# Performance work log

Measured on AMD Instinct MI355X. Metric: run time of the kernel, lower is better.

The kernel has to match this reference:

```python
import jax, jax.numpy as jnp
import numpy as np
import math

E = 512
H = 2048
P = 128  # attention_limit

def _make_params(key):
    ks = jax.random.split(key, 6)
    s = 0.02
    p = {}
    p['wq'] = jax.random.normal(ks[0], (E, E), jnp.float32) * s
    p['bq'] = jnp.zeros((E,), jnp.float32)
    p['wk'] = jax.random.normal(ks[1], (E, E), jnp.float32) * s
    p['bk'] = jnp.zeros((E,), jnp.float32)
    p['wv'] = jax.random.normal(ks[2], (E, E), jnp.float32) * s
    p['bv'] = jnp.zeros((E,), jnp.float32)
    p['w1'] = jax.random.normal(ks[3], (E, H), jnp.float32) * s
    p['b1'] = jnp.zeros((H,), jnp.float32)
    p['w2'] = jax.random.normal(ks[4], (H, E), jnp.float32) * s
    p['b2'] = jnp.zeros((E,), jnp.float32)
    p['ln1_w'] = jnp.ones((E,), jnp.float32)
    p['ln1_b'] = jnp.zeros((E,), jnp.float32)
    p['ln2_w'] = jnp.ones((E,), jnp.float32)
    p['ln2_b'] = jnp.zeros((E,), jnp.float32)
    return p

def setup_inputs() -> dict:
    key = jax.random.key(0)
    kx, kp = jax.random.split(key)
    inp = {'x': jax.random.normal(kx, (2, 1024, E), jnp.float32)}
    inp.update(_make_params(kp))
    return inp

def _layernorm(x, w, b, eps=1e-5):
    mu = jnp.mean(x, axis=-1, keepdims=True)
    var = jnp.mean((x - mu) ** 2, axis=-1, keepdims=True)
    return (x - mu) / jnp.sqrt(var + eps) * w + b

def _forward(x, wq, bq, wk, bk, wv, bv, w1, b1, w2, b2, ln1_w, ln1_b, ln2_w, ln2_b):
    B, S, Ed = x.shape
    # "RoPE" is actually additive sinusoidal PE in the source
    pos = jnp.arange(S, dtype=jnp.float32)[:, None]
    div = jnp.exp(jnp.arange(0, Ed, 2, dtype=jnp.float32) * (-math.log(10000.0) / Ed))
    pe = jnp.zeros((S, Ed), jnp.float32)
    pe = pe.at[:, 0::2].set(jnp.sin(pos * div))
    pe = pe.at[:, 1::2].set(jnp.cos(pos * div))
    x = x + pe[None]

    # local attention: pad x first, then apply K/V linears (padded rows -> bias)
    x_ext = jnp.pad(x, ((0, 0), (P, P), (0, 0)))
    q = x @ wq + bq                      # [B,S,E]
    k_ext = x_ext @ wk + bk              # [B,S+2P,E]
    v_ext = x_ext @ wv + bv
    W = 2 * P + 1
    win_idx = jnp.arange(S)[:, None] + jnp.arange(W)[None, :]  # [S,W]
    k_win = k_ext[:, win_idx]            # [B,S,W,E]
    v_win = v_ext[:, win_idx]            # [B,S,W,E]
    energy = jnp.einsum('bse,bswe->bsw', q, k_win) / jnp.sqrt(jnp.float32(Ed))
    attn = jax.nn.softmax(energy, axis=-1)
    attn_out = jnp.einsum('bsw,bswe->bse', attn, v_win)

    x = _layernorm(attn_out + x, ln1_w, ln1_b)
    ff = jnp.maximum(x @ w1 + b1, 0.0) @ w2 + b2
    return _layernorm(ff + x, ln2_w, ln2_b)

def reference(x, wq, bq, wk, bk, wv, bv, w1, b1, w2, b2, ln1_w, ln1_b, ln2_w, ln2_b):
    return _forward(x, wq, bq, wk, bk, wv, bv, w1, b1, w2, b2, ln1_w, ln1_b, ln2_w, ln2_b)
```

## Files before the change

### kernel.cpp

```cpp
#include <hip/hip_runtime.h>
#include <hip/hip_bf16.h>

#define S_LEN 1024
#define E_DIM 512
#define H_DIM 2048
#define P_PAD 128
#define EXTA 1296
#define BS_ROWS 2048

typedef __attribute__((ext_vector_type(8))) short bf16x8;
typedef __attribute__((ext_vector_type(4))) float f32x4;

__device__ inline ushort f2bf(float x) {
  union { float f; unsigned u; } c; c.f = x;
  unsigned u = c.u;
  u += 0x7fffu + ((u >> 16) & 1u);
  return (ushort)(u >> 16);
}

__device__ inline void gload16(ushort* dst, const ushort* src) {
  __builtin_amdgcn_global_load_lds(
      (const __attribute__((address_space(1))) void*)src,
      (__attribute__((address_space(3))) void*)dst, 16, 0, 0);
}

__global__ __launch_bounds__(256) void prep_kernel(const float* __restrict__ x,
                                                   const float* __restrict__ bk,
                                                   const float* __restrict__ bv,
                                                   const float* __restrict__ wq,
                                                   const float* __restrict__ wk,
                                                   const float* __restrict__ wv,
                                                   const float* __restrict__ w1,
                                                   const float* __restrict__ w2,
                                                   float* __restrict__ xpe,
                                                   ushort* __restrict__ xpe_bf,
                                                   ushort* __restrict__ k_bf,
                                                   ushort* __restrict__ v_t,
                                                   ushort* __restrict__ wqkvT,
                                                   ushort* __restrict__ w1T,
                                                   ushort* __restrict__ w2T) {
  __shared__ float t[32][33];
  const int blk = blockIdx.x;
  if (blk < 4096) {
    int idx = blk * 256 + threadIdx.x;
    int e = idx & (E_DIM - 1);
    int s = (idx >> 9) & (S_LEN - 1);
    const float c = -9.210340371976184f / 512.0f;
    float freq = expf((float)(e & ~1) * c);
    float ang = (float)s * freq;
    float pe = (e & 1) ? cosf(ang) : sinf(ang);
    float v = x[idx] + pe;
    xpe[idx] = v;
    xpe_bf[idx] = f2bf(v);
  } else if (blk < 6272) {
    int p = (blk - 4096) * 256 + threadIdx.x;
    int t2 = p / (2 * 272 * 512);
    int r2 = p % (2 * 272 * 512);
    int b = r2 / (272 * 512);
    int r3 = r2 % (272 * 512);
    if (t2 == 0) {
      int rr = r3 >> 9, e = r3 & 511;
      int row = rr < 128 ? rr : 1024 + rr;
      float v = rr < 256 ? bk[e] : 0.f;
      k_bf[((size_t)b * EXTA + row) * 512 + e] = f2bf(v);
    } else {
      int n = r3 / 272, jj = r3 % 272;
      int j = jj < 128 ? jj : 1024 + jj;
      float v = jj < 256 ? bv[n] : 0.f;
      v_t[((size_t)b * 512 + n) * EXTA + j] = f2bf(v);
    }
  } else {
    const int tile = blk - 6272;
    const float* W; ushort* WT; int K, N, bx, by;
    if (tile < 768) {
      K = 512; N = 512;
      int sect = tile >> 8, tt = tile & 255;
      W = sect == 0 ? wq : (sect == 1 ? wk : wv);
      WT = wqkvT + (size_t)sect * 512 * 512;
      bx = tt & 15; by = tt >> 4;
    } else if (tile < 1792) {
      K = 512; N = 2048; W = w1; WT = w1T;
      int tt = tile - 768; bx = tt & 63; by = tt >> 6;
    } else {
      K = 2048; N = 512; W = w2; WT = w2T;
      int tt = tile - 1792; bx = tt & 15; by = tt >> 4;
    }
    int lx = threadIdx.x & 31, ly = threadIdx.x >> 5;
    int n0 = bx * 32, k0 = by * 32;
#pragma unroll
    for (int r = 0; r < 4; ++r)
      t[ly + r * 8][lx] = W[(size_t)(k0 + ly + r * 8) * N + n0 + lx];
    __syncthreads();
#pragma unroll
    for (int r = 0; r < 4; ++r)
      WT[(size_t)(n0 + ly + r * 8) * K + k0 + lx] = f2bf(t[lx][ly + r * 8]);
  }
}

template <int BM, int BN, int WM, int WN, int OUT>
__global__ __launch_bounds__(256) void mfma_gemm(const ushort* __restrict__ A,
                                                 const ushort* __restrict__ Bt,
                                                 const float* __restrict__ bias,
                                                 const float* __restrict__ bias2,
                                                 const float* __restrict__ bias3,
                                                 void* __restrict__ Cout,
                                                 ushort* __restrict__ q_out,
                                                 ushort* __restrict__ k_out,
                                                 ushort* __restrict__ v_out,
                                                 int M, int N, int K, int LDA) {
  constexpr int WAVES_N = BN / WN;
  constexpr int FM = WM / 16, FN = WN / 16;
  __shared__ ushort As[BM * 64];
  __shared__ ushort Bs[BN * 64];
  const int tid = threadIdx.x;
  const int lane = tid & 63;
  const int w = tid >> 6;
  const int wr = w / WAVES_N, wc = w % WAVES_N;
  const int l15 = lane & 15, lhi = lane >> 4;
  const int col0 = blockIdx.x * BN, row0 = blockIdx.y * BM;
  const int koff = blockIdx.z * K;

  f32x4 acc[FM][FN] = {};

  for (int k0 = 0; k0 < K; k0 += 64) {
#pragma unroll
    for (int it = 0; it < BM / 32; ++it) {
      int u = it * 256 + tid;
      int r = u >> 3;
      int c16 = (u & 7) ^ (r & 7);
      gload16(&As[(size_t)u * 8], &A[(size_t)(row0 + r) * LDA + koff + k0 + c16 * 8]);
    }
#pragma unroll
    for (int it = 0; it < BN / 32; ++it) {
      int u = it * 256 + tid;
      int r = u >> 3;
      int c16 = (u & 7) ^ (r & 7);
      gload16(&Bs[(size_t)u * 8], &Bt[(size_t)(col0 + r) * LDA + koff + k0 + c16 * 8]);
    }
    __syncthreads();
#pragma unroll
    for (int kk = 0; kk < 2; ++kk) {
      bf16x8 af[FM], bfr[FN];
#pragma unroll
      for (int mi = 0; mi < FM; ++mi) {
        int r = wr * WM + mi * 16 + l15;
        int c16 = (kk * 4 + lhi) ^ (r & 7);
        af[mi] = *(const bf16x8*)&As[r * 64 + c16 * 8];
      }
#pragma unroll
      for (int ni = 0; ni < FN; ++ni) {
        int r = wc * WN + ni * 16 + l15;
        int c16 = (kk * 4 + lhi) ^ (r & 7);
        bfr[ni] = *(const bf16x8*)&Bs[r * 64 + c16 * 8];
      }
#pragma unroll
      for (int mi = 0; mi < FM; ++mi)
#pragma unroll
        for (int ni = 0; ni < FN; ++ni)
          acc[mi][ni] = __builtin_amdgcn_mfma_f32_16x16x32_bf16(af[mi], bfr[ni], acc[mi][ni], 0, 0, 0);
    }
    __syncthreads();
  }

#pragma unroll
  for (int mi = 0; mi < FM; ++mi) {
    int mbase = row0 + wr * WM + mi * 16 + lhi * 4;
#pragma unroll
    for (int ni = 0; ni < FN; ++ni) {
      int n = col0 + wc * WN + ni * 16 + l15;
      if constexpr (OUT == 1) {
        float b = bias[n];
        ushort* C = (ushort*)Cout;
#pragma unroll
        for (int j = 0; j < 4; ++j) C[(size_t)(mbase + j) * N + n] = f2bf(fmaxf(acc[mi][ni][j] + b, 0.f));
      } else if constexpr (OUT == 3) {
        float* C = (float*)Cout + (size_t)blockIdx.z * M * N;
#pragma unroll
        for (int j = 0; j < 4; ++j) C[(size_t)(mbase + j) * N + n] = acc[mi][ni][j];
      } else {
        int sect = n >> 9, nn = n & 511;
        float b = sect == 0 ? bias[nn] : (sect == 1 ? bias2[nn] : bias3[nn]);
        int bb = mbase >> 10;
        int s = mbase & 1023;
        if (sect == 0) {
#pragma unroll
          for (int j = 0; j < 4; ++j) q_out[(size_t)(mbase + j) * 512 + nn] = f2bf(acc[mi][ni][j] + b);
        } else if (sect == 1) {
#pragma unroll
          for (int j = 0; j < 4; ++j)
            k_out[((size_t)bb * EXTA + 128 + s + j) * 512 + nn] = f2bf(acc[mi][ni][j] + b);
        } else {
          ushort4 pk;
          pk.x = f2bf(acc[mi][ni][0] + b);
          pk.y = f2bf(acc[mi][ni][1] + b);
          pk.z = f2bf(acc[mi][ni][2] + b);
          pk.w = f2bf(acc[mi][ni][3] + b);
          *(ushort4*)&v_out[((size_t)bb * 512 + nn) * EXTA + 128 + s] = pk;
        }
      }
    }
  }
}

__global__ __launch_bounds__(512) void attn_ln1(const ushort* __restrict__ qb,
                                                const ushort* __restrict__ kb,
                                                const ushort* __restrict__ vt,
                                                const float* __restrict__ x_pe,
                                                const float* __restrict__ ln1w,
                                                const float* __restrict__ ln1b,
                                                float* __restrict__ x1,
                                                ushort* __restrict__ x1bf) {
  __shared__ float e_s[16][292];
  __shared__ ushort p_s[16][296];
  __shared__ float inv_s[16];
  __shared__ float redS[8][16];
  __shared__ float redQ[8][16];
  __shared__ float mu_s[16], rs_s[16];
  const int tid = threadIdx.x;
  const int lane = tid & 63;
  const int w = tid >> 6;
  const int l15 = lane & 15, lhi = lane >> 4;
  const int tile = blockIdx.x;
  const int b = tile >> 6;
  const int s0 = (tile & 63) * 16;
  const int base0 = b * 1024 + s0;

  const ushort* qrow = qb + (size_t)(base0 + l15) * 512 + lhi * 8;
  bf16x8 qf[16];
#pragma unroll
  for (int ks = 0; ks < 16; ++ks) qf[ks] = *(const bf16x8*)(qrow + ks * 32);

  const float scale = 0.044194173824159216f;
  const ushort* kbase = kb + (size_t)b * EXTA * 512 + (size_t)(s0 + l15) * 512 + lhi * 8;

  for (int jt = w; jt < 18; jt += 8) {
    f32x4 acc = {};
    const ushort* kp = kbase + (size_t)jt * 16 * 512;
#pragma unroll
    for (int ks = 0; ks < 16; ++ks) {
      bf16x8 kf = *(const bf16x8*)(kp + ks * 32);
      acc = __builtin_amdgcn_mfma_f32_16x16x32_bf16(qf[ks], kf, acc, 0, 0, 0);
    }
    int jc = jt * 16 + l15;
#pragma unroll
    for (int j = 0; j < 4; ++j) {
      int i = lhi * 4 + j;
      bool valid = (jc >= i) && (jc <= i + 256);
      e_s[i][jc] = valid ? acc[j] * scale : -1e30f;
    }
  }
  __syncthreads();

  {
    int r = tid >> 5, c0 = tid & 31;
    float m = -1e30f;
#pragma unroll
    for (int t = 0; t < 9; ++t) m = fmaxf(m, e_s[r][c0 + 32 * t]);
#pragma unroll
    for (int off = 1; off <= 16; off <<= 1) m = fmaxf(m, __shfl_xor(m, off));
    float s = 0.f;
#pragma unroll
    for (int t = 0; t < 9; ++t) {
      float p = __expf(e_s[r][c0 + 32 * t] - m);
      s += p;
      p_s[r][c0 + 32 * t] = f2bf(p);
    }
#pragma unroll
    for (int off = 1; off <= 16; off <<= 1) s += __shfl_xor(s, off);
    if (c0 == 0) inv_s[r] = 1.0f / s;
  }
  __syncthreads();

  bf16x8 pf[9];
#pragma unroll
  for (int ks = 0; ks < 9; ++ks) pf[ks] = *(const bf16x8*)&p_s[l15][ks * 32 + lhi * 8];
  float inv[4];
#pragma unroll
  for (int j = 0; j < 4; ++j) inv[j] = inv_s[lhi * 4 + j];

  const ushort* vbase = vt + (size_t)b * 512 * EXTA + s0 + lhi * 8;
  float val[4][4];
#pragma unroll
  for (int ni = 0; ni < 4; ++ni) {
    int n = w * 64 + ni * 16 + l15;
    f32x4 acc = {};
    const ushort* vp = vbase + (size_t)n * EXTA;
#pragma unroll
    for (int ks = 0; ks < 9; ++ks) {
      bf16x8 vf = *(const bf16x8*)(vp + ks * 32);
      acc = __builtin_amdgcn_mfma_f32_16x16x32_bf16(pf[ks], vf, acc, 0, 0, 0);
    }
#pragma unroll
    for (int j = 0; j < 4; ++j) {
      int r = lhi * 4 + j;
      val[ni][j] = acc[j] * inv[j] + x_pe[(size_t)(base0 + r) * 512 + n];
    }
  }

  float S[4], Q[4];
#pragma unroll
  for (int j = 0; j < 4; ++j) {
    S[j] = 0.f; Q[j] = 0.f;
#pragma unroll
    for (int ni = 0; ni < 4; ++ni) { S[j] += val[ni][j]; Q[j] += val[ni][j] * val[ni][j]; }
  }
#pragma unroll
  for (int off = 1; off <= 8; off <<= 1) {
#pragma unroll
    for (int j = 0; j < 4; ++j) {
      S[j] += __shfl_xor(S[j], off);
      Q[j] += __shfl_xor(Q[j], off);
    }
  }
  if (l15 == 0) {
#pragma unroll
    for (int j = 0; j < 4; ++j) { redS[w][lhi * 4 + j] = S[j]; redQ[w][lhi * 4 + j] = Q[j]; }
  }
  __syncthreads();
  if (tid < 16) {
    float sS = 0.f, sQ = 0.f;
#pragma unroll
    for (int ww = 0; ww < 8; ++ww) { sS += redS[ww][tid]; sQ += redQ[ww][tid]; }
    float mu = sS * (1.0f / 512.0f);
    float var = sQ * (1.0f / 512.0f) - mu * mu;
    mu_s[tid] = mu;
    rs_s[tid] = rsqrtf(var + 1e-5f);
  }
  __syncthreads();

#pragma unroll
  for (int ni = 0; ni < 4; ++ni) {
    int n = w * 64 + ni * 16 + l15;
    float lw = ln1w[n], lb = ln1b[n];
#pragma unroll
    for (int j = 0; j < 4; ++j) {
      int r = lhi * 4 + j;
      float o = (val[ni][j] - mu_s[r]) * rs_s[r] * lw + lb;
      x1[(size_t)(base0 + r) * 512 + n] = o;
      x1bf[(size_t)(base0 + r) * 512 + n] = f2bf(o);
    }
  }
}

__device__ inline float wave_reduce_sum(float v) {
#pragma unroll
  for (int off = 32; off >= 1; off >>= 1) v += __shfl_xor(v, off);
  return v;
}

__global__ __launch_bounds__(256) void ln_kernel(const float* __restrict__ a,
                                                 const float* __restrict__ a2,
                                                 const float* __restrict__ ab,
                                                 const float* __restrict__ rsd,
                                                 const float* __restrict__ w,
                                                 const float* __restrict__ bias,
                                                 float* __restrict__ out) {
  const int row = blockIdx.x;
  const int tid = threadIdx.x;
  __shared__ float red[8];
  const int e0 = tid * 2;
  const size_t base = (size_t)row * E_DIM + e0;
  float2 av = *(const float2*)(a + base);
  float2 rv = *(const float2*)(rsd + base);
  float x0 = av.x + rv.x, x1 = av.y + rv.y;
  {
    float2 v2 = *(const float2*)(a2 + base);
    x0 += v2.x; x1 += v2.y;
  }
  {
    float2 bb = *(const float2*)(ab + e0);
    x0 += bb.x; x1 += bb.y;
  }

  float sm = wave_reduce_sum(x0 + x1);
  if ((tid & 63) == 0) red[tid >> 6] = sm;
  __syncthreads();
  float mu = (red[0] + red[1] + red[2] + red[3]) * (1.0f / 512.0f);
  float d0 = x0 - mu, d1 = x1 - mu;
  float vs = wave_reduce_sum(d0 * d0 + d1 * d1);
  if ((tid & 63) == 0) red[4 + (tid >> 6)] = vs;
  __syncthreads();
  float var = (red[4] + red[5] + red[6] + red[7]) * (1.0f / 512.0f);
  float inv = rsqrtf(var + 1e-5f);
  float2 wv = *(const float2*)(w + e0);
  float2 bi = *(const float2*)(bias + e0);
  float o0 = d0 * inv * wv.x + bi.x;
  float o1 = d1 * inv * wv.y + bi.y;
  *(float2*)(out + base) = make_float2(o0, o1);
}

extern "C" void kernel_launch(void* const* d_in, const int* in_sizes, int n_in,
                              void* d_out, int out_size, void* d_ws, size_t ws_size,
                              hipStream_t stream) {
  const float* x    = (const float*)d_in[0];
  const float* wq   = (const float*)d_in[1];
  const float* bq   = (const float*)d_in[2];
  const float* wk   = (const float*)d_in[3];
  const float* bk   = (const float*)d_in[4];
  const float* wv   = (const float*)d_in[5];
  const float* bv   = (const float*)d_in[6];
  const float* w1   = (const float*)d_in[7];
  const float* b1   = (const float*)d_in[8];
  const float* w2   = (const float*)d_in[9];
  const float* b2   = (const float*)d_in[10];
  const float* ln1w = (const float*)d_in[11];
  const float* ln1b = (const float*)d_in[12];
  const float* ln2w = (const float*)d_in[13];
  const float* ln2b = (const float*)d_in[14];

  char* W = (char*)d_ws;
  float*  x_pe   = (float*)(W);
  ushort* xpebf  = (ushort*)(W + (4u  << 20));
  ushort* wqkvT  = (ushort*)(W + (6u  << 20));
  ushort* w1T    = (ushort*)(W + (8u  << 20));
  ushort* w2T    = (ushort*)(W + (10u << 20));
  ushort* q_bf   = (ushort*)(W + (12u << 20));
  ushort* k_bf   = (ushort*)(W + (14u << 20));
  ushort* v_t    = (ushort*)(W + (17u << 20));
  float*  x1     = (float*)(W + (20u << 20));
  ushort* x1bf   = (ushort*)(W + (24u << 20));
  ushort* ff1_bf = (ushort*)(W + (26u << 20));
  float*  ff2    = (float*)(W + (34u << 20));

  prep_kernel<<<9088, 256, 0, stream>>>(x, bk, bv, wq, wk, wv, w1, w2,
                                        x_pe, xpebf, k_bf, v_t, wqkvT, w1T, w2T);

  mfma_gemm<64, 128, 32, 64, 2><<<dim3(12, 32), 256, 0, stream>>>(
      xpebf, wqkvT, bq, bk, bv, nullptr, q_bf, k_bf, v_t, BS_ROWS, 1536, 512, 512);

  attn_ln1<<<128, 512, 0, stream>>>(q_bf, k_bf, v_t, x_pe, ln1w, ln1b, x1, x1bf);

  mfma_gemm<64, 128, 32, 64, 1><<<dim3(16, 32), 256, 0, stream>>>(
      x1bf, w1T, b1, nullptr, nullptr, ff1_bf, nullptr, nullptr, nullptr, BS_ROWS, H_DIM, 512, 512);

  mfma_gemm<64, 64, 32, 32, 3><<<dim3(8, 32, 2), 256, 0, stream>>>(
      ff1_bf, w2T, nullptr, nullptr, nullptr, ff2, nullptr, nullptr, nullptr, BS_ROWS, E_DIM, 1024, 2048);

  ln_kernel<<<BS_ROWS, 256, 0, stream>>>(ff2, ff2 + (size_t)BS_ROWS * E_DIM, b2, x1,
                                         ln2w, ln2b, (float*)d_out);
}
```

Measured before the change: 77.08 us.

## Fuse all stages into one cooperative persistent kernel with grid syncs

Replaces the six separate launches (prep, QKV GEMM, attention+LN1, FF1 GEMM, FF2 GEMM, LN2) with a single cooperative kernel of 256 blocks of 512 threads that separates phases with grid.sync(). GEMM tiles grow to 128x128, and FF2 is split over four K-slices instead of two, with the final LayerNorm reducing those partials one row per wave. The aim is to remove launch gaps and inter-kernel overhead, at the cost of grid-wide barriers, idle blocks in phases with fewer tiles (QKV uses 192 blocks, attention 128), and a fixed small grid.

```diff
diff --git a/kernel.cpp b/kernel.cpp
--- a/kernel.cpp
+++ b/kernel.cpp
@@ -1,10 +1,12 @@
 #include <hip/hip_runtime.h>
 #include <hip/hip_bf16.h>
+#include <hip/hip_cooperative_groups.h>
+
+namespace cg = cooperative_groups;
 
 #define S_LEN 1024
 #define E_DIM 512
 #define H_DIM 2048
-#define P_PAD 128
 #define EXTA 1296
 #define BS_ROWS 2048
 
@@ -24,157 +26,98 @@
       (__attribute__((address_space(3))) void*)dst, 16, 0, 0);
 }
 
-__global__ __launch_bounds__(256) void prep_kernel(const float* __restrict__ x,
-                                                   const float* __restrict__ bk,
-                                                   const float* __restrict__ bv,
-                                                   const float* __restrict__ wq,
-                                                   const float* __restrict__ wk,
-                                                   const float* __restrict__ wv,
-                                                   const float* __restrict__ w1,
-                                                   const float* __restrict__ w2,
-                                                   float* __restrict__ xpe,
-                                                   ushort* __restrict__ xpe_bf,
-                                                   ushort* __restrict__ k_bf,
-                                                   ushort* __restrict__ v_t,
-                                                   ushort* __restrict__ wqkvT,
-                                                   ushort* __restrict__ w1T,
-                                                   ushort* __restrict__ w2T) {
-  __shared__ float t[32][33];
-  const int blk = blockIdx.x;
-  if (blk < 4096) {
-    int idx = blk * 256 + threadIdx.x;
-    int e = idx & (E_DIM - 1);
-    int s = (idx >> 9) & (S_LEN - 1);
-    const float c = -9.210340371976184f / 512.0f;
-    float freq = expf((float)(e & ~1) * c);
-    float ang = (float)s * freq;
-    float pe = (e & 1) ? cosf(ang) : sinf(ang);
-    float v = x[idx] + pe;
-    xpe[idx] = v;
-    xpe_bf[idx] = f2bf(v);
-  } else if (blk < 6272) {
-    int p = (blk - 4096) * 256 + threadIdx.x;
-    int t2 = p / (2 * 272 * 512);
-    int r2 = p % (2 * 272 * 512);
-    int b = r2 / (272 * 512);
-    int r3 = r2 % (272 * 512);
-    if (t2 == 0) {
-      int rr = r3 >> 9, e = r3 & 511;
-      int row = rr < 128 ? rr : 1024 + rr;
-      float v = rr < 256 ? bk[e] : 0.f;
-      k_bf[((size_t)b * EXTA + row) * 512 + e] = f2bf(v);
-    } else {
-      int n = r3 / 272, jj = r3 % 272;
-      int j = jj < 128 ? jj : 1024 + jj;
-      float v = jj < 256 ? bv[n] : 0.f;
-      v_t[((size_t)b * 512 + n) * EXTA + j] = f2bf(v);
-    }
-  } else {
-    const int tile = blk - 6272;
-    const float* W; ushort* WT; int K, N, bx, by;
-    if (tile < 768) {
-      K = 512; N = 512;
-      int sect = tile >> 8, tt = tile & 255;
-      W = sect == 0 ? wq : (sect == 1 ? wk : wv);
-      WT = wqkvT + (size_t)sect * 512 * 512;
-      bx = tt & 15; by = tt >> 4;
-    } else if (tile < 1792) {
-      K = 512; N = 2048; W = w1; WT = w1T;
-      int tt = tile - 768; bx = tt & 63; by = tt >> 6;
-    } else {
-      K = 2048; N = 512; W = w2; WT = w2T;
-      int tt = tile - 1792; bx = tt & 15; by = tt >> 4;
-    }
-    int lx = threadIdx.x & 31, ly = threadIdx.x >> 5;
-    int n0 = bx * 32, k0 = by * 32;
-#pragma unroll
-    for (int r = 0; r < 4; ++r)
-      t[ly + r * 8][lx] = W[(size_t)(k0 + ly + r * 8) * N + n0 + lx];
-    __syncthreads();
-#pragma unroll
-    for (int r = 0; r < 4; ++r)
-      WT[(size_t)(n0 + ly + r * 8) * K + k0 + lx] = f2bf(t[lx][ly + r * 8]);
-  }
-}
-
-template <int BM, int BN, int WM, int WN, int OUT>
-__global__ __launch_bounds__(256) void mfma_gemm(const ushort* __restrict__ A,
-                                                 const ushort* __restrict__ Bt,
-                                                 const float* __restrict__ bias,
-                                                 const float* __restrict__ bias2,
-                                                 const float* __restrict__ bias3,
-                                                 void* __restrict__ Cout,
-                                                 ushort* __restrict__ q_out,
-                                                 ushort* __restrict__ k_out,
-                                                 ushort* __restrict__ v_out,
-                                                 int M, int N, int K, int LDA) {
-  constexpr int WAVES_N = BN / WN;
-  constexpr int FM = WM / 16, FN = WN / 16;
-  __shared__ ushort As[BM * 64];
-  __shared__ ushort Bs[BN * 64];
+struct Params {
+  const float *x, *bq, *bk, *bv, *b1, *b2, *ln1w, *ln1b, *ln2w, *ln2b;
+  const float *wq, *wk, *wv, *w1, *w2;
+  float *x_pe, *x1, *ff2, *out;
+  ushort *xpebf, *wqkvT, *w1T, *w2T, *q_bf, *k_bf, *v_t, *x1bf, *ff1_bf;
+};
+
+union SMem {
+  struct { ushort As[128 * 64]; ushort Bs[128 * 64]; } g;
+  struct {
+    float e[16][292];
+    ushort p[16][296];
+    float inv[16];
+    float redS[8][16];
+    float redQ[8][16];
+    float mu[16];
+    float rs[16];
+  } a;
+  struct { float t[2][32][33]; } tr;
+};
+
+template <int OUT>
+__device__ __forceinline__ void gemm_tile(ushort* As, ushort* Bs,
+                                          const ushort* __restrict__ A,
+                                          const ushort* __restrict__ Bt,
+                                          int row0, int col0, int koff,
+                                          int ldaA, int ldaB, int N,
+                                          const float* bias, const float* bias2,
+                                          const float* bias3, void* Cout,
+                                          ushort* q_out, ushort* k_out, ushort* v_out,
+                                          size_t zoff) {
   const int tid = threadIdx.x;
   const int lane = tid & 63;
   const int w = tid >> 6;
-  const int wr = w / WAVES_N, wc = w % WAVES_N;
+  const int wr = w >> 2, wc = w & 3;
   const int l15 = lane & 15, lhi = lane >> 4;
-  const int col0 = blockIdx.x * BN, row0 = blockIdx.y * BM;
-  const int koff = blockIdx.z * K;
-
-  f32x4 acc[FM][FN] = {};
-
-  for (int k0 = 0; k0 < K; k0 += 64) {
-#pragma unroll
-    for (int it = 0; it < BM / 32; ++it) {
-      int u = it * 256 + tid;
+  f32x4 acc[4][2] = {};
+
+  for (int k0 = 0; k0 < 512; k0 += 64) {
+#pragma unroll
+    for (int it = 0; it < 2; ++it) {
+      int u = it * 512 + tid;
       int r = u >> 3;
       int c16 = (u & 7) ^ (r & 7);
-      gload16(&As[(size_t)u * 8], &A[(size_t)(row0 + r) * LDA + koff + k0 + c16 * 8]);
-    }
-#pragma unroll
-    for (int it = 0; it < BN / 32; ++it) {
-      int u = it * 256 + tid;
+      gload16(&As[u * 8], &A[(size_t)(row0 + r) * ldaA + koff + k0 + c16 * 8]);
+    }
+#pragma unroll
+    for (int it = 0; it < 2; ++it) {
+      int u = it * 512 + tid;
       int r = u >> 3;
       int c16 = (u & 7) ^ (r & 7);
-      gload16(&Bs[(size_t)u * 8], &Bt[(size_t)(col0 + r) * LDA + koff + k0 + c16 * 8]);
+      gload16(&Bs[u * 8], &Bt[(size_t)(col0 + r) * ldaB + koff + k0 + c16 * 8]);
     }
     __syncthreads();
 #pragma unroll
     for (int kk = 0; kk < 2; ++kk) {
-      bf16x8 af[FM], bfr[FN];
-#pragma unroll
-      for (int mi = 0; mi < FM; ++mi) {
-        int r = wr * WM + mi * 16 + l15;
+      bf16x8 af[4], bfv[2];
+#pragma unroll
+      for (int mi = 0; mi < 4; ++mi) {
+        int r = wr * 64 + mi * 16 + l15;
         int c16 = (kk * 4 + lhi) ^ (r & 7);
         af[mi] = *(const bf16x8*)&As[r * 64 + c16 * 8];
       }
 #pragma unroll
-      for (int ni = 0; ni < FN; ++ni) {
-        int r = wc * WN + ni * 16 + l15;
+      for (int ni = 0; ni < 2; ++ni) {
+        int r = wc * 32 + ni * 16 + l15;
         int c16 = (kk * 4 + lhi) ^ (r & 7);
-        bfr[ni] = *(const bf16x8*)&Bs[r * 64 + c16 * 8];
-      }
-#pragma unroll
-      for (int mi = 0; mi < FM; ++mi)
-#pragma unroll
-        for (int ni = 0; ni < FN; ++ni)
-          acc[mi][ni] = __builtin_amdgcn_mfma_f32_16x16x32_bf16(af[mi], bfr[ni], acc[mi][ni], 0, 0, 0);
-    }
-    __syncthreads();
-  }
-
-#pragma unroll
-  for (int mi = 0; mi < FM; ++mi) {
-    int mbase = row0 + wr * WM + mi * 16 + lhi * 4;
-#pragma unroll
-    for (int ni = 0; ni < FN; ++ni) {
-      int n = col0 + wc * WN + ni * 16 + l15;
+        bfv[ni] = *(const bf16x8*)&Bs[r * 64 + c16 * 8];
+      }
+#pragma unroll
+      for (int mi = 0; mi < 4; ++mi)
+#pragma unroll
+        for (int ni = 0; ni < 2; ++ni)
+          acc[mi][ni] = __builtin_amdgcn_mfma_f32_16x16x32_bf16(af[mi], bfv[ni], acc[mi][ni], 0, 0, 0);
+    }
+    __syncthreads();
+  }
+
+#pragma unroll
+  for (int mi = 0; mi < 4; ++mi) {
+    int mbase = row0 + wr * 64 + mi * 16 + lhi * 4;
+#pragma unroll
+    for (int ni = 0; ni < 2; ++ni) {
+      int n = col0 + wc * 32 + ni * 16 + l15;
       if constexpr (OUT == 1) {
         float b = bias[n];
         ushort* C = (ushort*)Cout;
 #pragma unroll
-        for (int j = 0; j < 4; ++j) C[(size_t)(mbase + j) * N + n] = f2bf(fmaxf(acc[mi][ni][j] + b, 0.f));
+        for (int j = 0; j < 4; ++j)
+          C[(size_t)(mbase + j) * N + n] = f2bf(fmaxf(acc[mi][ni][j] + b, 0.f));
       } else if constexpr (OUT == 3) {
-        float* C = (float*)Cout + (size_t)blockIdx.z * M * N;
+        float* C = (float*)Cout + zoff;
 #pragma unroll
         for (int j = 0; j < 4; ++j) C[(size_t)(mbase + j) * N + n] = acc[mi][ni][j];
       } else {
@@ -184,7 +127,8 @@
         int s = mbase & 1023;
         if (sect == 0) {
 #pragma unroll
-          for (int j = 0; j < 4; ++j) q_out[(size_t)(mbase + j) * 512 + nn] = f2bf(acc[mi][ni][j] + b);
+          for (int j = 0; j < 4; ++j)
+            q_out[(size_t)(mbase + j) * 512 + nn] = f2bf(acc[mi][ni][j] + b);
         } else if (sect == 1) {
 #pragma unroll
           for (int j = 0; j < 4; ++j)
@@ -202,240 +146,321 @@
   }
 }
 
-__global__ __launch_bounds__(512) void attn_ln1(const ushort* __restrict__ qb,
-                                                const ushort* __restrict__ kb,
-                                                const ushort* __restrict__ vt,
-                                                const float* __restrict__ x_pe,
-                                                const float* __restrict__ ln1w,
-                                                const float* __restrict__ ln1b,
-                                                float* __restrict__ x1,
-                                                ushort* __restrict__ x1bf) {
-  __shared__ float e_s[16][292];
-  __shared__ ushort p_s[16][296];
-  __shared__ float inv_s[16];
-  __shared__ float redS[8][16];
-  __shared__ float redQ[8][16];
-  __shared__ float mu_s[16], rs_s[16];
+__global__ __launch_bounds__(512, 2) void mega_kernel(Params p) {
+  cg::grid_group grid = cg::this_grid();
+  __shared__ SMem sm;
+  const int bid = blockIdx.x;
   const int tid = threadIdx.x;
   const int lane = tid & 63;
   const int w = tid >> 6;
   const int l15 = lane & 15, lhi = lane >> 4;
-  const int tile = blockIdx.x;
-  const int b = tile >> 6;
-  const int s0 = (tile & 63) * 16;
-  const int base0 = b * 1024 + s0;
-
-  const ushort* qrow = qb + (size_t)(base0 + l15) * 512 + lhi * 8;
-  bf16x8 qf[16];
-#pragma unroll
-  for (int ks = 0; ks < 16; ++ks) qf[ks] = *(const bf16x8*)(qrow + ks * 32);
-
-  const float scale = 0.044194173824159216f;
-  const ushort* kbase = kb + (size_t)b * EXTA * 512 + (size_t)(s0 + l15) * 512 + lhi * 8;
-
-  for (int jt = w; jt < 18; jt += 8) {
-    f32x4 acc = {};
-    const ushort* kp = kbase + (size_t)jt * 16 * 512;
-#pragma unroll
-    for (int ks = 0; ks < 16; ++ks) {
-      bf16x8 kf = *(const bf16x8*)(kp + ks * 32);
-      acc = __builtin_amdgcn_mfma_f32_16x16x32_bf16(qf[ks], kf, acc, 0, 0, 0);
-    }
-    int jc = jt * 16 + l15;
+
+  {
+    const int sub = tid >> 8;
+    const int t256 = tid & 255;
+    for (int iter = 0; iter < 18; ++iter) {
+      int j = iter * 512 + bid * 2 + sub;
+      bool isT = (j >= 6272 && j < 9088);
+      const float* Wsrc = nullptr; ushort* WT = nullptr; int K = 0, N = 0, bx = 0, by = 0;
+      if (j < 4096) {
+        int idx = j * 256 + t256;
+        int e = idx & (E_DIM - 1);
+        int s = (idx >> 9) & (S_LEN - 1);
+        const float c = -9.210340371976184f / 512.0f;
+        float freq = expf((float)(e & ~1) * c);
+        float ang = (float)s * freq;
+        float pe = (e & 1) ? cosf(ang) : sinf(ang);
+        float v = p.x[idx] + pe;
+        p.x_pe[idx] = v;
+        p.xpebf[idx] = f2bf(v);
+      } else if (j < 6272) {
+        int pp = (j - 4096) * 256 + t256;
+        int t2 = pp / (2 * 272 * 512);
+        int r2 = pp % (2 * 272 * 512);
+        int b = r2 / (272 * 512);
+        int r3 = r2 % (272 * 512);
+        if (t2 == 0) {
+          int rr = r3 >> 9, e = r3 & 511;
+          int row = rr < 128 ? rr : 1024 + rr;
+          float v = rr < 256 ? p.bk[e] : 0.f;
+          p.k_bf[((size_t)b * EXTA + row) * 512 + e] = f2bf(v);
+        } else {
+          int n = r3 / 272, jj = r3 % 272;
+          int col = jj < 128 ? jj : 1024 + jj;
+          float v = jj < 256 ? p.bv[n] : 0.f;
+          p.v_t[((size_t)b * 512 + n) * EXTA + col] = f2bf(v);
+        }
+      } else if (isT) {
+        int tile = j - 6272;
+        if (tile < 768) {
+          K = 512; N = 512;
+          int sect = tile >> 8, tt = tile & 255;
+          Wsrc = sect == 0 ? p.wq : (sect == 1 ? p.wk : p.wv);
+          WT = p.wqkvT + (size_t)sect * 512 * 512;
+          bx = tt & 15; by = tt >> 4;
+        } else if (tile < 1792) {
+          K = 512; N = 2048; Wsrc = p.w1; WT = p.w1T;
+          int tt = tile - 768; bx = tt & 63; by = tt >> 6;
+        } else {
+          K = 2048; N = 512; Wsrc = p.w2; WT = p.w2T;
+          int tt = tile - 1792; bx = tt & 15; by = tt >> 4;
+        }
+        int lx = t256 & 31, ly = t256 >> 5;
+        int n0 = bx * 32, k0 = by * 32;
+#pragma unroll
+        for (int r = 0; r < 4; ++r)
+          sm.tr.t[sub][ly + r * 8][lx] = Wsrc[(size_t)(k0 + ly + r * 8) * N + n0 + lx];
+      }
+      __syncthreads();
+      if (isT) {
+        int lx = t256 & 31, ly = t256 >> 5;
+        int n0 = bx * 32, k0 = by * 32;
+#pragma unroll
+        for (int r = 0; r < 4; ++r)
+          WT[(size_t)(n0 + ly + r * 8) * K + k0 + lx] = f2bf(sm.tr.t[sub][lx][ly + r * 8]);
+      }
+      __syncthreads();
+    }
+  }
+  grid.sync();
+
+  if (bid < 192) {
+    int trow = bid / 12, tcol = bid % 12;
+    gemm_tile<2>(sm.g.As, sm.g.Bs, p.xpebf, p.wqkvT, trow * 128, tcol * 128, 0,
+                 512, 512, 1536, p.bq, p.bk, p.bv, nullptr, p.q_bf, p.k_bf, p.v_t, 0);
+  }
+  grid.sync();
+
+  if (bid < 128) {
+    const int b = bid >> 6;
+    const int s0 = (bid & 63) * 16;
+    const int base0 = b * 1024 + s0;
+
+    const ushort* qrow = p.q_bf + (size_t)(base0 + l15) * 512 + lhi * 8;
+    bf16x8 qf[16];
+#pragma unroll
+    for (int ks = 0; ks < 16; ++ks) qf[ks] = *(const bf16x8*)(qrow + ks * 32);
+
+    const float scale = 0.044194173824159216f;
+    const ushort* kbase = p.k_bf + (size_t)b * EXTA * 512 + (size_t)(s0 + l15) * 512 + lhi * 8;
+
+    for (int jt = w; jt < 18; jt += 8) {
+      f32x4 acc = {};
+      const ushort* kp = kbase + (size_t)jt * 16 * 512;
+#pragma unroll
+      for (int ks = 0; ks < 16; ++ks) {
+        bf16x8 kf = *(const bf16x8*)(kp + ks * 32);
+        acc = __builtin_amdgcn_mfma_f32_16x16x32_bf16(qf[ks], kf, acc, 0, 0, 0);
+      }
+      int jc = jt * 16 + l15;
+#pragma unroll
+      for (int j = 0; j < 4; ++j) {
+        int i = lhi * 4 + j;
+        bool valid = (jc >= i) && (jc <= i + 256);
+        sm.a.e[i][jc] = valid ? acc[j] * scale : -1e30f;
+      }
+    }
+    __syncthreads();
+
+    {
+      int r = tid >> 5, c0 = tid & 31;
+      float m = -1e30f;
+#pragma unroll
+      for (int t = 0; t < 9; ++t) m = fmaxf(m, sm.a.e[r][c0 + 32 * t]);
+#pragma unroll
+      for (int off = 1; off <= 16; off <<= 1) m = fmaxf(m, __shfl_xor(m, off));
+      float s = 0.f;
+#pragma unroll
+      for (int t = 0; t < 9; ++t) {
+        float pv = __expf(sm.a.e[r][c0 + 32 * t] - m);
+        s += pv;
+        sm.a.p[r][c0 + 32 * t] = f2bf(pv);
+      }
+#pragma unroll
+      for (int off = 1; off <= 16; off <<= 1) s += __shfl_xor(s, off);
+      if (c0 == 0) sm.a.inv[r] = 1.0f / s;
+    }
+    __syncthreads();
+
+    bf16x8 pf[9];
+#pragma unroll
+    for (int ks = 0; ks < 9; ++ks) pf[ks] = *(const bf16x8*)&sm.a.p[l15][ks * 32 + lhi * 8];
+    float inv[4];
+#pragma unroll
+    for (int j = 0; j < 4; ++j) inv[j] = sm.a.inv[lhi * 4 + j];
+
+    const ushort* vbase = p.v_t + (size_t)b * 512 * EXTA + s0 + lhi * 8;
+    float val[4][4];
+#pragma unroll
+    for (int ni = 0; ni < 4; ++ni) {
+      int n = w * 64 + ni * 16 + l15;
+      f32x4 acc = {};
+      const ushort* vp = vbase + (size_t)n * EXTA;
+#pragma unroll
+      for (int ks = 0; ks < 9; ++ks) {
+        bf16x8 vf = *(const bf16x8*)(vp + ks * 32);
+        acc = __builtin_amdgcn_mfma_f32_16x16x32_bf16(pf[ks], vf, acc, 0, 0, 0);
+      }
+#pragma unroll
+      for (int j = 0; j < 4; ++j) {
+        int r = lhi * 4 + j;
+        val[ni][j] = acc[j] * inv[j] + p.x_pe[(size_t)(base0 + r) * 512 + n];
+      }
+    }
+
+    float S[4], Q[4];
 #pragma unroll
     for (int j = 0; j < 4; ++j) {
-      int i = lhi * 4 + j;
-      bool valid = (jc >= i) && (jc <= i + 256);
-      e_s[i][jc] = valid ? acc[j] * scale : -1e30f;
-    }
-  }
-  __syncthreads();
+      S[j] = 0.f; Q[j] = 0.f;
+#pragma unroll
+      for (int ni = 0; ni < 4; ++ni) { S[j] += val[ni][j]; Q[j] += val[ni][j] * val[ni][j]; }
+    }
+#pragma unroll
+    for (int off = 1; off <= 8; off <<= 1) {
+#pragma unroll
+      for (int j = 0; j < 4; ++j) {
+        S[j] += __shfl_xor(S[j], off);
+        Q[j] += __shfl_xor(Q[j], off);
+      }
+    }
+    if (l15 == 0) {
+#pragma unroll
+      for (int j = 0; j < 4; ++j) { sm.a.redS[w][lhi * 4 + j] = S[j]; sm.a.redQ[w][lhi * 4 + j] = Q[j]; }
+    }
+    __syncthreads();
+    if (tid < 16) {
+      float sS = 0.f, sQ = 0.f;
+#pragma unroll
+      for (int ww = 0; ww < 8; ++ww) { sS += sm.a.redS[ww][tid]; sQ += sm.a.redQ[ww][tid]; }
+      float mu = sS * (1.0f / 512.0f);
+      float var = sQ * (1.0f / 512.0f) - mu * mu;
+      sm.a.mu[tid] = mu;
+      sm.a.rs[tid] = rsqrtf(var + 1e-5f);
+    }
+    __syncthreads();
+
+#pragma unroll
+    for (int ni = 0; ni < 4; ++ni) {
+      int n = w * 64 + ni * 16 + l15;
+      float lw = p.ln1w[n], lb = p.ln1b[n];
+#pragma unroll
+      for (int j = 0; j < 4; ++j) {
+        int r = lhi * 4 + j;
+        float o = (val[ni][j] - sm.a.mu[r]) * sm.a.rs[r] * lw + lb;
+        p.x1[(size_t)(base0 + r) * 512 + n] = o;
+        p.x1bf[(size_t)(base0 + r) * 512 + n] = f2bf(o);
+      }
+    }
+  }
+  grid.sync();
 
   {
-    int r = tid >> 5, c0 = tid & 31;
-    float m = -1e30f;
-#pragma unroll
-    for (int t = 0; t < 9; ++t) m = fmaxf(m, e_s[r][c0 + 32 * t]);
-#pragma unroll
-    for (int off = 1; off <= 16; off <<= 1) m = fmaxf(m, __shfl_xor(m, off));
-    float s = 0.f;
-#pragma unroll
-    for (int t = 0; t < 9; ++t) {
-      float p = __expf(e_s[r][c0 + 32 * t] - m);
-      s += p;
-      p_s[r][c0 + 32 * t] = f2bf(p);
-    }
-#pragma unroll
-    for (int off = 1; off <= 16; off <<= 1) s += __shfl_xor(s, off);
-    if (c0 == 0) inv_s[r] = 1.0f / s;
-  }
-  __syncthreads();
-
-  bf16x8 pf[9];
-#pragma unroll
-  for (int ks = 0; ks < 9; ++ks) pf[ks] = *(const bf16x8*)&p_s[l15][ks * 32 + lhi * 8];
-  float inv[4];
-#pragma unroll
-  for (int j = 0; j < 4; ++j) inv[j] = inv_s[lhi * 4 + j];
-
-  const ushort* vbase = vt + (size_t)b * 512 * EXTA + s0 + lhi * 8;
-  float val[4][4];
-#pragma unroll
-  for (int ni = 0; ni < 4; ++ni) {
-    int n = w * 64 + ni * 16 + l15;
-    f32x4 acc = {};
-    const ushort* vp = vbase + (size_t)n * EXTA;
-#pragma unroll
-    for (int ks = 0; ks < 9; ++ks) {
-      bf16x8 vf = *(const bf16x8*)(vp + ks * 32);
-      acc = __builtin_amdgcn_mfma_f32_16x16x32_bf16(pf[ks], vf, acc, 0, 0, 0);
-    }
-#pragma unroll
-    for (int j = 0; j < 4; ++j) {
-      int r = lhi * 4 + j;
-      val[ni][j] = acc[j] * inv[j] + x_pe[(size_t)(base0 + r) * 512 + n];
-    }
-  }
-
-  float S[4], Q[4];
-#pragma unroll
-  for (int j = 0; j < 4; ++j) {
-    S[j] = 0.f; Q[j] = 0.f;
-#pragma unroll
-    for (int ni = 0; ni < 4; ++ni) { S[j] += val[ni][j]; Q[j] += val[ni][j] * val[ni][j]; }
-  }
-#pragma unroll
-  for (int off = 1; off <= 8; off <<= 1) {
-#pragma unroll
-    for (int j = 0; j < 4; ++j) {
-      S[j] += __shfl_xor(S[j], off);
-      Q[j] += __shfl_xor(Q[j], off);
-    }
-  }
-  if (l15 == 0) {
-#pragma unroll
-    for (int j = 0; j < 4; ++j) { redS[w][lhi * 4 + j] = S[j]; redQ[w][lhi * 4 + j] = Q[j]; }
-  }
-  __syncthreads();
-  if (tid < 16) {
-    float sS = 0.f, sQ = 0.f;
-#pragma unroll
-    for (int ww = 0; ww < 8; ++ww) { sS += redS[ww][tid]; sQ += redQ[ww][tid]; }
-    float mu = sS * (1.0f / 512.0f);
-    float var = sQ * (1.0f / 512.0f) - mu * mu;
-    mu_s[tid] = mu;
-    rs_s[tid] = rsqrtf(var + 1e-5f);
-  }
-  __syncthreads();
-
-#pragma unroll
-  for (int ni = 0; ni < 4; ++ni) {
-    int n = w * 64 + ni * 16 + l15;
-    float lw = ln1w[n], lb = ln1b[n];
-#pragma unroll
-    for (int j = 0; j < 4; ++j) {
-      int r = lhi * 4 + j;
-      float o = (val[ni][j] - mu_s[r]) * rs_s[r] * lw + lb;
-      x1[(size_t)(base0 + r) * 512 + n] = o;
-      x1bf[(size_t)(base0 + r) * 512 + n] = f2bf(o);
-    }
-  }
-}
-
-__device__ inline float wave_reduce_sum(float v) {
-#pragma unroll
-  for (int off = 32; off >= 1; off >>= 1) v += __shfl_xor(v, off);
-  return v;
-}
-
-__global__ __launch_bounds__(256) void ln_kernel(const float* __restrict__ a,
-                                                 const float* __restrict__ a2,
-                                                 const float* __restrict__ ab,
-                                                 const float* __restrict__ rsd,
-                                                 const float* __restrict__ w,
-                                                 const float* __restrict__ bias,
-                                                 float* __restrict__ out) {
-  const int row = blockIdx.x;
-  const int tid = threadIdx.x;
-  __shared__ float red[8];
-  const int e0 = tid * 2;
-  const size_t base = (size_t)row * E_DIM + e0;
-  float2 av = *(const float2*)(a + base);
-  float2 rv = *(const float2*)(rsd + base);
-  float x0 = av.x + rv.x, x1 = av.y + rv.y;
+    int trow = bid >> 4, tcol = bid & 15;
+    gemm_tile<1>(sm.g.As, sm.g.Bs, p.x1bf, p.w1T, trow * 128, tcol * 128, 0,
+                 512, 512, 2048, p.b1, nullptr, nullptr, p.ff1_bf, nullptr, nullptr, nullptr, 0);
+  }
+  grid.sync();
+
   {
-    float2 v2 = *(const float2*)(a2 + base);
-    x0 += v2.x; x1 += v2.y;
-  }
+    int slice = bid >> 6, tt = bid & 63;
+    int trow = tt >> 2, tcol = tt & 3;
+    gemm_tile<3>(sm.g.As, sm.g.Bs, p.ff1_bf, p.w2T, trow * 128, tcol * 128, slice * 512,
+                 2048, 2048, 512, nullptr, nullptr, nullptr, p.ff2, nullptr, nullptr, nullptr,
+                 (size_t)slice * BS_ROWS * 512);
+  }
+  grid.sync();
+
   {
-    float2 bb = *(const float2*)(ab + e0);
-    x0 += bb.x; x1 += bb.y;
-  }
-
-  float sm = wave_reduce_sum(x0 + x1);
-  if ((tid & 63) == 0) red[tid >> 6] = sm;
-  __syncthreads();
-  float mu = (red[0] + red[1] + red[2] + red[3]) * (1.0f / 512.0f);
-  float d0 = x0 - mu, d1 = x1 - mu;
-  float vs = wave_reduce_sum(d0 * d0 + d1 * d1);
-  if ((tid & 63) == 0) red[4 + (tid >> 6)] = vs;
-  __syncthreads();
-  float var = (red[4] + red[5] + red[6] + red[7]) * (1.0f / 512.0f);
-  float inv = rsqrtf(var + 1e-5f);
-  float2 wv = *(const float2*)(w + e0);
-  float2 bi = *(const float2*)(bias + e0);
-  float o0 = d0 * inv * wv.x + bi.x;
-  float o1 = d1 * inv * wv.y + bi.y;
-  *(float2*)(out + base) = make_float2(o0, o1);
+    int r = bid * 8 + w;
+    int c0 = lane * 8;
+    float v[8];
+    const float* pa = p.ff2 + (size_t)r * 512 + c0;
+    {
+      const float4* q4 = (const float4*)pa;
+      float4 a = q4[0], bq4 = q4[1];
+      v[0] = a.x; v[1] = a.y; v[2] = a.z; v[3] = a.w;
+      v[4] = bq4.x; v[5] = bq4.y; v[6] = bq4.z; v[7] = bq4.w;
+    }
+#pragma unroll
+    for (int s = 1; s < 4; ++s) {
+      const float4* q4 = (const float4*)(pa + (size_t)s * BS_ROWS * 512);
+      float4 a = q4[0], bq4 = q4[1];
+      v[0] += a.x; v[1] += a.y; v[2] += a.z; v[3] += a.w;
+      v[4] += bq4.x; v[5] += bq4.y; v[6] += bq4.z; v[7] += bq4.w;
+    }
+    {
+      const float4* bb = (const float4*)(p.b2 + c0);
+      float4 a = bb[0], b4 = bb[1];
+      v[0] += a.x; v[1] += a.y; v[2] += a.z; v[3] += a.w;
+      v[4] += b4.x; v[5] += b4.y; v[6] += b4.z; v[7] += b4.w;
+      const float4* xr = (const float4*)(p.x1 + (size_t)r * 512 + c0);
+      float4 c = xr[0], d = xr[1];
+      v[0] += c.x; v[1] += c.y; v[2] += c.z; v[3] += c.w;
+      v[4] += d.x; v[5] += d.y; v[6] += d.z; v[7] += d.w;
+    }
+    float S = 0.f, Q = 0.f;
+#pragma unroll
+    for (int j = 0; j < 8; ++j) { S += v[j]; Q += v[j] * v[j]; }
+#pragma unroll
+    for (int off = 1; off <= 32; off <<= 1) { S += __shfl_xor(S, off); Q += __shfl_xor(Q, off); }
+    float mu = S * (1.0f / 512.0f);
+    float var = Q * (1.0f / 512.0f) - mu * mu;
+    float rs = rsqrtf(var + 1e-5f);
+    const float4* lw4 = (const float4*)(p.ln2w + c0);
+    const float4* lb4 = (const float4*)(p.ln2b + c0);
+    float4 w0 = lw4[0], w1v = lw4[1], b0 = lb4[0], b1v = lb4[1];
+    float ow[8] = {w0.x, w0.y, w0.z, w0.w, w1v.x, w1v.y, w1v.z, w1v.w};
+    float ob[8] = {b0.x, b0.y, b0.z, b0.w, b1v.x, b1v.y, b1v.z, b1v.w};
+    float4 o0, o1;
+    o0.x = (v[0] - mu) * rs * ow[0] + ob[0];
+    o0.y = (v[1] - mu) * rs * ow[1] + ob[1];
+    o0.z = (v[2] - mu) * rs * ow[2] + ob[2];
+    o0.w = (v[3] - mu) * rs * ow[3] + ob[3];
+    o1.x = (v[4] - mu) * rs * ow[4] + ob[4];
+    o1.y = (v[5] - mu) * rs * ow[5] + ob[5];
+    o1.z = (v[6] - mu) * rs * ow[6] + ob[6];
+    o1.w = (v[7] - mu) * rs * ow[7] + ob[7];
+    float* op = p.out + (size_t)r * 512 + c0;
+    ((float4*)op)[0] = o0;
+    ((float4*)op)[1] = o1;
+  }
 }
 
 extern "C" void kernel_launch(void* const* d_in, const int* in_sizes, int n_in,
                               void* d_out, int out_size, void* d_ws, size_t ws_size,
                               hipStream_t stream) {
-  const float* x    = (const float*)d_in[0];
-  const float* wq   = (const float*)d_in[1];
-  const float* bq   = (const float*)d_in[2];
-  const float* wk   = (const float*)d_in[3];
-  const float* bk   = (const float*)d_in[4];
-  const float* wv   = (const float*)d_in[5];
-  const float* bv   = (const float*)d_in[6];
-  const float* w1   = (const float*)d_in[7];
-  const float* b1   = (const float*)d_in[8];
-  const float* w2   = (const float*)d_in[9];
-  const float* b2   = (const float*)d_in[10];
-  const float* ln1w = (const float*)d_in[11];
-  const float* ln1b = (const float*)d_in[12];
-  const float* ln2w = (const float*)d_in[13];
-  const float* ln2b = (const float*)d_in[14];
-
   char* W = (char*)d_ws;
-  float*  x_pe   = (float*)(W);
-  ushort* xpebf  = (ushort*)(W + (4u  << 20));
-  ushort* wqkvT  = (ushort*)(W + (6u  << 20));
-  ushort* w1T    = (ushort*)(W + (8u  << 20));
-  ushort* w2T    = (ushort*)(W + (10u << 20));
-  ushort* q_bf   = (ushort*)(W + (12u << 20));
-  ushort* k_bf   = (ushort*)(W + (14u << 20));
-  ushort* v_t    = (ushort*)(W + (17u << 20));
-  float*  x1     = (float*)(W + (20u << 20));
-  ushort* x1bf   = (ushort*)(W + (24u << 20));
-  ushort* ff1_bf = (ushort*)(W + (26u << 20));
-  float*  ff2    = (float*)(W + (34u << 20));
-
-  prep_kernel<<<9088, 256, 0, stream>>>(x, bk, bv, wq, wk, wv, w1, w2,
-                                        x_pe, xpebf, k_bf, v_t, wqkvT, w1T, w2T);
-
-  mfma_gemm<64, 128, 32, 64, 2><<<dim3(12, 32), 256, 0, stream>>>(
-      xpebf, wqkvT, bq, bk, bv, nullptr, q_bf, k_bf, v_t, BS_ROWS, 1536, 512, 512);
-
-  attn_ln1<<<128, 512, 0, stream>>>(q_bf, k_bf, v_t, x_pe, ln1w, ln1b, x1, x1bf);
-
-  mfma_gemm<64, 128, 32, 64, 1><<<dim3(16, 32), 256, 0, stream>>>(
-      x1bf, w1T, b1, nullptr, nullptr, ff1_bf, nullptr, nullptr, nullptr, BS_ROWS, H_DIM, 512, 512);
-
-  mfma_gemm<64, 64, 32, 32, 3><<<dim3(8, 32, 2), 256, 0, stream>>>(
-      ff1_bf, w2T, nullptr, nullptr, nullptr, ff2, nullptr, nullptr, nullptr, BS_ROWS, E_DIM, 1024, 2048);
-
-  ln_kernel<<<BS_ROWS, 256, 0, stream>>>(ff2, ff2 + (size_t)BS_ROWS * E_DIM, b2, x1,
-                                         ln2w, ln2b, (float*)d_out);
+  Params p;
+  p.x    = (const float*)d_in[0];
+  p.wq   = (const float*)d_in[1];
+  p.bq   = (const float*)d_in[2];
+  p.wk   = (const float*)d_in[3];
+  p.bk   = (const float*)d_in[4];
+  p.wv   = (const float*)d_in[5];
+  p.bv   = (const float*)d_in[6];
+  p.w1   = (const float*)d_in[7];
+  p.b1   = (const float*)d_in[8];
+  p.w2   = (const float*)d_in[9];
+  p.b2   = (const float*)d_in[10];
+  p.ln1w = (const float*)d_in[11];
+  p.ln1b = (const float*)d_in[12];
+  p.ln2w = (const float*)d_in[13];
+  p.ln2b = (const float*)d_in[14];
+
+  p.x_pe   = (float*)(W);
+  p.xpebf  = (ushort*)(W + (4u  << 20));
+  p.wqkvT  = (ushort*)(W + (6u  << 20));
+  p.w1T    = (ushort*)(W + (8u  << 20));
+  p.w2T    = (ushort*)(W + (10u << 20));
+  p.q_bf   = (ushort*)(W + (12u << 20));
+  p.k_bf   = (ushort*)(W + (14u << 20));
+  p.v_t    = (ushort*)(W + (17u << 20));
+  p.x1     = (float*)(W + (20u << 20));
+  p.x1bf   = (ushort*)(W + (24u << 20));
+  p.ff1_bf = (ushort*)(W + (26u << 20));
+  p.ff2    = (float*)(W + (34u << 20));
+  p.out    = (float*)d_out;
+
+  void* args[] = {&p};
+  hipLaunchCooperativeKernel((void*)mega_kernel, dim3(256), dim3(512), args, 0, stream);
 }
```

After: 250.9 us. 3.26x slower.
